# Kernel optimization log

Hardware: AMD Instinct MI355X
Metric: run time of the kernel (lower is better)

## Reference

```python
import jax, jax.numpy as jnp
import numpy as np
from jax import lax


def setup_inputs() -> dict:
    key = jax.random.key(0)
    ks = jax.random.split(key, 6)
    B, L, D, H, K = 32, 256, 16, 64, 5
    T = L - K + 1            # 252
    S = (T // 2) * H         # 8064
    return {
        "x": jax.random.normal(ks[0], (B, L, D), dtype=jnp.float32),
        "conv_w": jax.random.normal(ks[1], (D, H, K), dtype=jnp.float32) * 0.1,
        "conv_b": jax.random.normal(ks[2], (D, H), dtype=jnp.float32) * 0.1,
        "deconv_w": jax.random.normal(ks[3], (D, H, K), dtype=jnp.float32) * 0.1,
        "deconv_b": jax.random.normal(ks[4], (D,), dtype=jnp.float32) * 0.1,
        "W_attn": jax.random.normal(ks[5], (S, S), dtype=jnp.float32) * 0.01,
    }


def reference(x, conv_w, conv_b, deconv_w, deconv_b, W_attn):
    B, L, D = x.shape
    _, H, K = conv_w.shape
    T = L - K + 1
    P = T // 2
    S = P * H

    xt = jnp.transpose(x, (0, 2, 1))  # [B, D, L]
    # per-channel Conv1d(1->H) as one grouped conv: kernel [D*H, 1, K], groups=D
    y = lax.conv_general_dilated(
        xt, conv_w.reshape(D * H, 1, K), (1,), "VALID",
        dimension_numbers=("NCH", "OIH", "NCH"), feature_group_count=D,
    ) + conv_b.reshape(1, D * H, 1)
    y = jax.nn.relu(y)  # [B, D*H, T]

    # per-channel ConvTranspose1d(H->1) == full conv with flipped kernel, groups=D
    recon = lax.conv_general_dilated(
        y, deconv_w[..., ::-1], (1,), [(K - 1, K - 1)],
        dimension_numbers=("NCH", "OIH", "NCH"), feature_group_count=D,
    ) + deconv_b.reshape(1, D, 1)  # [B, D, L]

    # AvgPool1d(kernel=2, stride=2) then flatten(H, P) per channel
    pooled = y.reshape(B, D, H, P, 2).mean(axis=-1)  # [B, D, H, P]
    flat = pooled.reshape(B, D, S)                   # [B, D, S]

    main = flat[:, 0]        # [B, S]
    aux = flat[:, 1:]        # [B, D-1, S]

    # 'general' score: main . (aux @ W^T)  ==  (main @ W) . aux
    m = main @ W_attn                              # [B, S]
    scores = jnp.einsum("bt,bdt->bd", m, aux)      # [B, D-1]
    attn = jax.nn.softmax(scores, axis=-1)         # [B, D-1]
    weighted = jnp.einsum("bd,bds->bs", attn, aux)  # [B, S]

    out = jnp.concatenate([main[:, None, :], weighted[:, None, :]], axis=2)  # [B,1,2S]
    return out, attn[:, None, :], recon
```

## Files before the change

kernel.cpp:

```cpp
#include <hip/hip_runtime.h>
#include <math.h>

#define BB 32
#define LL 256
#define DD 16
#define HH 64
#define KK 5
#define TT 252
#define PP 126
#define SS 8064
#define NCHUNK 12
#define CHUNK 672
#define NKT 21

typedef __attribute__((ext_vector_type(8))) short bf16x8;
typedef __attribute__((ext_vector_type(4))) float f32x4;

__device__ __forceinline__ unsigned short f2bf(float f) {
  unsigned int u = __float_as_uint(f);
  u += 0x7FFFu + ((u >> 16) & 1u);
  return (unsigned short)(u >> 16);
}
__device__ __forceinline__ float bf2f(unsigned short h) {
  return __uint_as_float(((unsigned int)h) << 16);
}

__global__ __launch_bounds__(256) void k12_conv_recon(
    const float* __restrict__ x, const float* __restrict__ cw,
    const float* __restrict__ cb, const float* __restrict__ dw,
    const float* __restrict__ db, float* __restrict__ flat,
    unsigned short* __restrict__ mainH, unsigned short* __restrict__ mainL,
    float* __restrict__ recon) {
  __shared__ float ylds[HH * TT];
  __shared__ float xs[LL];
  __shared__ float cws[HH * KK];
  __shared__ float dws[HH * KK];
  __shared__ float cbs[HH];

  int bd = blockIdx.x;
  int b = bd / DD, d = bd % DD;
  int tid = threadIdx.x;

  xs[tid] = x[((size_t)b * LL + tid) * DD + d];
  for (int i = tid; i < HH * KK; i += 256) {
    cws[i] = cw[(size_t)d * HH * KK + i];
    dws[i] = dw[(size_t)d * HH * KK + i];
  }
  if (tid < HH) cbs[tid] = cb[d * HH + tid];
  __syncthreads();

  {
    int h = tid >> 2, a = tid & 3;
    int t0 = a * 63;
    float w0 = cws[h * KK + 0], w1 = cws[h * KK + 1], w2 = cws[h * KK + 2],
          w3 = cws[h * KK + 3], w4 = cws[h * KK + 4];
    float bias = cbs[h];
    float x0 = xs[t0], x1 = xs[t0 + 1], x2 = xs[t0 + 2], x3 = xs[t0 + 3],
          x4 = xs[t0 + 4];
    float* yrow = ylds + h * TT + t0;
    #pragma unroll 7
    for (int t = 0; t < 63; ++t) {
      float yv = fmaf(w4, x4, fmaf(w3, x3, fmaf(w2, x2, fmaf(w1, x1, fmaf(w0, x0, bias)))));
      yrow[t] = fmaxf(yv, 0.f);
      x0 = x1; x1 = x2; x2 = x3; x3 = x4;
      if (t < 62) x4 = xs[t0 + t + 5];
    }
  }
  __syncthreads();

  for (int i = tid; i < HH * PP; i += 256) {
    int h = i / PP, p = i - h * PP;
    float pooled = 0.5f * (ylds[h * TT + 2 * p] + ylds[h * TT + 2 * p + 1]);
    flat[(size_t)bd * SS + i] = pooled;
    if (d == 0) {
      unsigned short hb = f2bf(pooled);
      mainH[(size_t)b * SS + i] = hb;
      mainL[(size_t)b * SS + i] = f2bf(pooled - bf2f(hb));
    }
  }

  {
    int l = tid;
    float acc = db[d];
    for (int h = 0; h < HH; ++h) {
      const float* yl = ylds + h * TT;
      #pragma unroll
      for (int j = 0; j < KK; ++j) {
        int t = l - j;
        if (t >= 0 && t < TT) acc = fmaf(yl[t], dws[h * KK + j], acc);
      }
    }
    recon[(size_t)bd * LL + l] = acc;
  }
}

__global__ __launch_bounds__(256) void k3_mfma(
    const float* __restrict__ W, const unsigned short* __restrict__ mainH,
    const unsigned short* __restrict__ mainL, float* __restrict__ partial) {
  __shared__ unsigned short AH[4 * 32 * 8];
  __shared__ unsigned short AL[4 * 32 * 8];
  __shared__ unsigned short BH[4 * 64 * 8];
  __shared__ unsigned short BL[4 * 64 * 8];

  int tid = threadIdx.x;
  int chunk = blockIdx.y;
  int s0 = chunk * CHUNK;
  int cb = blockIdx.x * 64;

  int lane = tid & 63;
  int wv = tid >> 6;
  int mr = wv & 1;
  int nt0 = (wv >> 1) * 2;

  f32x4 acc0 = {0.f, 0.f, 0.f, 0.f};
  f32x4 acc1 = {0.f, 0.f, 0.f, 0.f};

  int sc = tid & 63;
  int sg = tid >> 6;

  int aoff = (lane >> 4) * 256 + ((lane & 15) + 16 * mr) * 8;
  int b0off = (lane >> 4) * 512 + ((lane & 15) + 16 * nt0) * 8;
  int b1off = b0off + 16 * 8;

  #pragma unroll 1
  for (int kt = 0; kt < NKT; ++kt) {
    const float* wsrc = W + (size_t)(s0 + kt * 32 + sg * 8) * SS + cb + sc;
    bf16x8 vh, vl;
    #pragma unroll
    for (int j = 0; j < 8; ++j) {
      float f = wsrc[(size_t)j * SS];
      unsigned short h = f2bf(f);
      float rem = f - bf2f(h);
      vh[j] = (short)h;
      vl[j] = (short)f2bf(rem);
    }
    *(bf16x8*)&BH[sg * 512 + sc * 8] = vh;
    *(bf16x8*)&BL[sg * 512 + sc * 8] = vl;
    if (tid < 128) {
      int ab = tid >> 2;
      int aq = tid & 3;
      size_t off = (size_t)ab * SS + (size_t)(s0 + kt * 32 + aq * 8);
      *(bf16x8*)&AH[aq * 256 + ab * 8] = *(const bf16x8*)(mainH + off);
      *(bf16x8*)&AL[aq * 256 + ab * 8] = *(const bf16x8*)(mainL + off);
    }
    __syncthreads();
    bf16x8 ah = *(const bf16x8*)&AH[aoff];
    bf16x8 al = *(const bf16x8*)&AL[aoff];
    bf16x8 b0h = *(const bf16x8*)&BH[b0off];
    bf16x8 b0l = *(const bf16x8*)&BL[b0off];
    bf16x8 b1h = *(const bf16x8*)&BH[b1off];
    bf16x8 b1l = *(const bf16x8*)&BL[b1off];
    acc0 = __builtin_amdgcn_mfma_f32_16x16x32_bf16(ah, b0h, acc0, 0, 0, 0);
    acc0 = __builtin_amdgcn_mfma_f32_16x16x32_bf16(ah, b0l, acc0, 0, 0, 0);
    acc0 = __builtin_amdgcn_mfma_f32_16x16x32_bf16(al, b0h, acc0, 0, 0, 0);
    acc1 = __builtin_amdgcn_mfma_f32_16x16x32_bf16(ah, b1h, acc1, 0, 0, 0);
    acc1 = __builtin_amdgcn_mfma_f32_16x16x32_bf16(ah, b1l, acc1, 0, 0, 0);
    acc1 = __builtin_amdgcn_mfma_f32_16x16x32_bf16(al, b1h, acc1, 0, 0, 0);
    __syncthreads();
  }

  int row0 = mr * 16 + (lane >> 4) * 4;
  int col0 = cb + nt0 * 16 + (lane & 15);
  float* pp = partial + ((size_t)chunk * BB + row0) * SS + col0;
  pp[0 * (size_t)SS] = acc0[0];
  pp[1 * (size_t)SS] = acc0[1];
  pp[2 * (size_t)SS] = acc0[2];
  pp[3 * (size_t)SS] = acc0[3];
  pp += 16;
  pp[0 * (size_t)SS] = acc1[0];
  pp[1 * (size_t)SS] = acc1[1];
  pp[2 * (size_t)SS] = acc1[2];
  pp[3 * (size_t)SS] = acc1[3];
}

__global__ __launch_bounds__(256) void k3b_reduce(
    const float4* __restrict__ partial, float4* __restrict__ m) {
  int i = blockIdx.x * 256 + threadIdx.x;
  float4 s = make_float4(0.f, 0.f, 0.f, 0.f);
  #pragma unroll
  for (int c = 0; c < NCHUNK; ++c) {
    float4 v = partial[(size_t)c * (BB * SS / 4) + i];
    s.x += v.x; s.y += v.y; s.z += v.z; s.w += v.w;
  }
  m[i] = s;
}

__global__ __launch_bounds__(256) void k4_scores(
    const float* __restrict__ m, const float* __restrict__ flat,
    float* __restrict__ scores) {
  int bd = blockIdx.x;
  int b = bd / 15, dd = bd % 15;
  const float* mb = m + (size_t)b * SS;
  const float* ab = flat + ((size_t)b * DD + 1 + dd) * SS;
  float p = 0.f;
  for (int s = threadIdx.x; s < SS; s += 256) p = fmaf(mb[s], ab[s], p);
  #pragma unroll
  for (int o = 32; o; o >>= 1) p += __shfl_xor(p, o);
  __shared__ float red[4];
  if ((threadIdx.x & 63) == 0) red[threadIdx.x >> 6] = p;
  __syncthreads();
  if (threadIdx.x == 0) scores[bd] = red[0] + red[1] + red[2] + red[3];
}

__global__ __launch_bounds__(64) void k5_softmax(
    const float* __restrict__ scores, float* __restrict__ attn_out) {
  int b = blockIdx.x;
  int lane = threadIdx.x;
  float v = (lane < 15) ? scores[b * 15 + lane] : -INFINITY;
  float mx = v;
  #pragma unroll
  for (int o = 32; o; o >>= 1) mx = fmaxf(mx, __shfl_xor(mx, o));
  float e = (lane < 15) ? expf(v - mx) : 0.f;
  float sum = e;
  #pragma unroll
  for (int o = 32; o; o >>= 1) sum += __shfl_xor(sum, o);
  if (lane < 15) attn_out[b * 15 + lane] = e / sum;
}

__global__ __launch_bounds__(256) void k6_out(
    const float* __restrict__ flat, const float* __restrict__ attn,
    float* __restrict__ out) {
  int b = blockIdx.y;
  int s = blockIdx.x * 256 + threadIdx.x;
  if (s >= SS) return;
  const float* fb = flat + (size_t)b * DD * SS;
  out[(size_t)b * 2 * SS + s] = fb[s];
  float w = 0.f;
  #pragma unroll
  for (int d = 0; d < 15; ++d)
    w = fmaf(attn[b * 15 + d], fb[(size_t)(1 + d) * SS + s], w);
  out[(size_t)b * 2 * SS + SS + s] = w;
}

extern "C" void kernel_launch(void* const* d_in, const int* in_sizes, int n_in,
                              void* d_out, int out_size, void* d_ws, size_t ws_size,
                              hipStream_t stream) {
  const float* x        = (const float*)d_in[0];
  const float* conv_w   = (const float*)d_in[1];
  const float* conv_b   = (const float*)d_in[2];
  const float* deconv_w = (const float*)d_in[3];
  const float* deconv_b = (const float*)d_in[4];
  const float* W_attn   = (const float*)d_in[5];
  float* out = (float*)d_out;

  const size_t ATTN_OFF  = (size_t)BB * 2 * SS;
  const size_t RECON_OFF = ATTN_OFF + (size_t)BB * 15;

  float* ws      = (float*)d_ws;
  float* partial = ws;
  float* flat    = partial + (size_t)NCHUNK * BB * SS;
  unsigned short* mainH = (unsigned short*)(flat + (size_t)BB * DD * SS);
  unsigned short* mainL = mainH + (size_t)BB * SS;
  float* m       = (float*)(mainL + (size_t)BB * SS);
  float* scores  = m + (size_t)BB * SS;

  k12_conv_recon<<<dim3(BB * DD), dim3(256), 0, stream>>>(
      x, conv_w, conv_b, deconv_w, deconv_b, flat, mainH, mainL, out + RECON_OFF);

  k3_mfma<<<dim3(SS / 64, NCHUNK), dim3(256), 0, stream>>>(
      W_attn, mainH, mainL, partial);

  k3b_reduce<<<dim3((BB * SS / 4) / 256), dim3(256), 0, stream>>>(
      (const float4*)partial, (float4*)m);

  k4_scores<<<dim3(BB * 15), dim3(256), 0, stream>>>(m, flat, scores);

  k5_softmax<<<dim3(BB), dim3(64), 0, stream>>>(scores, out + ATTN_OFF);

  k6_out<<<dim3((SS + 255) / 256, BB), dim3(256), 0, stream>>>(
      flat, out + ATTN_OFF, out);
}
```

Baseline: 106.7 us.

## Double-buffer LDS and prefetch W tiles two steps ahead in MFMA GEMV kernel

Restructures the k3_mfma main loop into a software pipeline. The W and main tiles for step kt+2 are loaded into registers and the tile for kt+1 is converted and written into a second LDS buffer while MFMAs run on the current buffer, which removes one __syncthreads per iteration. The bf16 hi/lo split switches from round-to-nearest to truncation, which is cheaper but changes how the error is split between the two halves. It costs more LDS and registers to hold the in-flight tile.

```diff
diff --git a/kernel.cpp b/kernel.cpp
--- a/kernel.cpp
+++ b/kernel.cpp
@@ -97,15 +97,15 @@
 __global__ __launch_bounds__(256) void k3_mfma(
     const float* __restrict__ W, const unsigned short* __restrict__ mainH,
     const unsigned short* __restrict__ mainL, float* __restrict__ partial) {
-  __shared__ unsigned short AH[4 * 32 * 8];
-  __shared__ unsigned short AL[4 * 32 * 8];
-  __shared__ unsigned short BH[4 * 64 * 8];
-  __shared__ unsigned short BL[4 * 64 * 8];
+  __shared__ unsigned short AH[2][1024];
+  __shared__ unsigned short AL[2][1024];
+  __shared__ unsigned short BH[2][2048];
+  __shared__ unsigned short BL[2][2048];
 
   int tid = threadIdx.x;
   int chunk = blockIdx.y;
   int s0 = chunk * CHUNK;
-  int cb = blockIdx.x * 64;
+  int cbase = blockIdx.x * 64;
 
   int lane = tid & 63;
   int wv = tid >> 6;
@@ -118,49 +118,74 @@
   int sc = tid & 63;
   int sg = tid >> 6;
 
-  int aoff = (lane >> 4) * 256 + ((lane & 15) + 16 * mr) * 8;
+  int aoff  = (lane >> 4) * 256 + ((lane & 15) + 16 * mr) * 8;
   int b0off = (lane >> 4) * 512 + ((lane & 15) + 16 * nt0) * 8;
-  int b1off = b0off + 16 * 8;
+  int b1off = b0off + 128;
+
+  const float* wbase = W + (size_t)(s0 + sg * 8) * SS + cbase + sc;
+  int ab = tid >> 2, aq = tid & 3;
+  size_t abase = (size_t)ab * SS + (size_t)(s0 + aq * 8);
+
+  float f0, f1, f2, f3, f4, f5, f6, f7;
+  bf16x8 aHr, aLr;
+
+#define LOADW(KT) {                                                   \
+    const float* p_ = wbase + (size_t)(KT) * 32 * SS;                 \
+    f0 = p_[0];                f1 = p_[(size_t)SS];                   \
+    f2 = p_[2 * (size_t)SS];   f3 = p_[3 * (size_t)SS];               \
+    f4 = p_[4 * (size_t)SS];   f5 = p_[5 * (size_t)SS];               \
+    f6 = p_[6 * (size_t)SS];   f7 = p_[7 * (size_t)SS]; }
+
+#define LOADA(KT) if (tid < 128) {                                    \
+    aHr = *(const bf16x8*)(mainH + abase + (KT) * 32);                \
+    aLr = *(const bf16x8*)(mainL + abase + (KT) * 32); }
+
+#define SPLIT1(F, J) {                                                \
+    unsigned int u_ = __float_as_uint(F);                             \
+    vh[J] = (short)(u_ >> 16);                                        \
+    float rem_ = F - __uint_as_float(u_ & 0xFFFF0000u);               \
+    vl[J] = (short)(__float_as_uint(rem_) >> 16); }
+
+#define CVTW(BUF) {                                                   \
+    bf16x8 vh, vl;                                                    \
+    SPLIT1(f0, 0) SPLIT1(f1, 1) SPLIT1(f2, 2) SPLIT1(f3, 3)           \
+    SPLIT1(f4, 4) SPLIT1(f5, 5) SPLIT1(f6, 6) SPLIT1(f7, 7)           \
+    *(bf16x8*)&BH[BUF][sg * 512 + sc * 8] = vh;                       \
+    *(bf16x8*)&BL[BUF][sg * 512 + sc * 8] = vl; }
+
+#define WRITEA(BUF) if (tid < 128) {                                  \
+    *(bf16x8*)&AH[BUF][aq * 256 + ab * 8] = aHr;                      \
+    *(bf16x8*)&AL[BUF][aq * 256 + ab * 8] = aLr; }
+
+#define DOMFMA(BUF) {                                                 \
+    bf16x8 ah  = *(const bf16x8*)&AH[BUF][aoff];                      \
+    bf16x8 al  = *(const bf16x8*)&AL[BUF][aoff];                      \
+    bf16x8 b0h = *(const bf16x8*)&BH[BUF][b0off];                     \
+    bf16x8 b0l = *(const bf16x8*)&BL[BUF][b0off];                     \
+    bf16x8 b1h = *(const bf16x8*)&BH[BUF][b1off];                     \
+    bf16x8 b1l = *(const bf16x8*)&BL[BUF][b1off];                     \
+    acc0 = __builtin_amdgcn_mfma_f32_16x16x32_bf16(ah, b0h, acc0, 0, 0, 0); \
+    acc0 = __builtin_amdgcn_mfma_f32_16x16x32_bf16(ah, b0l, acc0, 0, 0, 0); \
+    acc0 = __builtin_amdgcn_mfma_f32_16x16x32_bf16(al, b0h, acc0, 0, 0, 0); \
+    acc1 = __builtin_amdgcn_mfma_f32_16x16x32_bf16(ah, b1h, acc1, 0, 0, 0); \
+    acc1 = __builtin_amdgcn_mfma_f32_16x16x32_bf16(ah, b1l, acc1, 0, 0, 0); \
+    acc1 = __builtin_amdgcn_mfma_f32_16x16x32_bf16(al, b1h, acc1, 0, 0, 0); }
+
+  LOADW(0) LOADA(0)
+  CVTW(0) WRITEA(0)
+  LOADW(1) LOADA(1)
+  __syncthreads();
 
   #pragma unroll 1
   for (int kt = 0; kt < NKT; ++kt) {
-    const float* wsrc = W + (size_t)(s0 + kt * 32 + sg * 8) * SS + cb + sc;
-    bf16x8 vh, vl;
-    #pragma unroll
-    for (int j = 0; j < 8; ++j) {
-      float f = wsrc[(size_t)j * SS];
-      unsigned short h = f2bf(f);
-      float rem = f - bf2f(h);
-      vh[j] = (short)h;
-      vl[j] = (short)f2bf(rem);
-    }
-    *(bf16x8*)&BH[sg * 512 + sc * 8] = vh;
-    *(bf16x8*)&BL[sg * 512 + sc * 8] = vl;
-    if (tid < 128) {
-      int ab = tid >> 2;
-      int aq = tid & 3;
-      size_t off = (size_t)ab * SS + (size_t)(s0 + kt * 32 + aq * 8);
-      *(bf16x8*)&AH[aq * 256 + ab * 8] = *(const bf16x8*)(mainH + off);
-      *(bf16x8*)&AL[aq * 256 + ab * 8] = *(const bf16x8*)(mainL + off);
-    }
+    DOMFMA(kt & 1)
+    if (kt + 1 < NKT) { CVTW((kt + 1) & 1) WRITEA((kt + 1) & 1) }
+    if (kt + 2 < NKT) { LOADW(kt + 2) LOADA(kt + 2) }
     __syncthreads();
-    bf16x8 ah = *(const bf16x8*)&AH[aoff];
-    bf16x8 al = *(const bf16x8*)&AL[aoff];
-    bf16x8 b0h = *(const bf16x8*)&BH[b0off];
-    bf16x8 b0l = *(const bf16x8*)&BL[b0off];
-    bf16x8 b1h = *(const bf16x8*)&BH[b1off];
-    bf16x8 b1l = *(const bf16x8*)&BL[b1off];
-    acc0 = __builtin_amdgcn_mfma_f32_16x16x32_bf16(ah, b0h, acc0, 0, 0, 0);
-    acc0 = __builtin_amdgcn_mfma_f32_16x16x32_bf16(ah, b0l, acc0, 0, 0, 0);
-    acc0 = __builtin_amdgcn_mfma_f32_16x16x32_bf16(al, b0h, acc0, 0, 0, 0);
-    acc1 = __builtin_amdgcn_mfma_f32_16x16x32_bf16(ah, b1h, acc1, 0, 0, 0);
-    acc1 = __builtin_amdgcn_mfma_f32_16x16x32_bf16(ah, b1l, acc1, 0, 0, 0);
-    acc1 = __builtin_amdgcn_mfma_f32_16x16x32_bf16(al, b1h, acc1, 0, 0, 0);
-    __syncthreads();
   }
 
   int row0 = mr * 16 + (lane >> 4) * 4;
-  int col0 = cb + nt0 * 16 + (lane & 15);
+  int col0 = cbase + nt0 * 16 + (lane & 15);
   float* pp = partial + ((size_t)chunk * BB + row0) * SS + col0;
   pp[0 * (size_t)SS] = acc0[0];
   pp[1 * (size_t)SS] = acc0[1];
@@ -171,6 +196,12 @@
   pp[1 * (size_t)SS] = acc1[1];
   pp[2 * (size_t)SS] = acc1[2];
   pp[3 * (size_t)SS] = acc1[3];
+#undef LOADW
+#undef LOADA
+#undef SPLIT1
+#undef CVTW
+#undef WRITEA
+#undef DOMFMA
 }
 
 __global__ __launch_bounds__(256) void k3b_reduce(
```

Result: faster. 101.0 us (-5.4%).

## Rewrite GEMV-style matmul as LDS-free per-wave 32x32 MFMA with register pipelining

Applied to the files above, without the earlier changes.

Each wavefront now owns a 32-column by 384-row slice of W and loads its operands straight from global memory into registers, removing the shared-memory staging and both block barriers per step. It switches to 32x32x16 bf16 MFMAs and software-pipelines loads three steps deep. The bf16 hi/lo split of W becomes truncation instead of round-to-nearest, which is cheaper and keeps the three-product split accurate. The split-K count grows from 12 to 21 chunks, so the reduce kernel reads more partial sums.

```diff
diff --git a/kernel.cpp b/kernel.cpp
--- a/kernel.cpp
+++ b/kernel.cpp
@@ -9,12 +9,13 @@
 #define TT 252
 #define PP 126
 #define SS 8064
-#define NCHUNK 12
-#define CHUNK 672
-#define NKT 21
+#define NCHUNK 21
+#define CHUNK 384
+#define NSTEP 24
+#define NCT 252
 
 typedef __attribute__((ext_vector_type(8))) short bf16x8;
-typedef __attribute__((ext_vector_type(4))) float f32x4;
+typedef __attribute__((ext_vector_type(16))) float f32x16;
 
 __device__ __forceinline__ unsigned short f2bf(float f) {
   unsigned int u = __float_as_uint(f);
@@ -97,80 +98,75 @@
 __global__ __launch_bounds__(256) void k3_mfma(
     const float* __restrict__ W, const unsigned short* __restrict__ mainH,
     const unsigned short* __restrict__ mainL, float* __restrict__ partial) {
-  __shared__ unsigned short AH[4 * 32 * 8];
-  __shared__ unsigned short AL[4 * 32 * 8];
-  __shared__ unsigned short BH[4 * 64 * 8];
-  __shared__ unsigned short BL[4 * 64 * 8];
-
   int tid = threadIdx.x;
-  int chunk = blockIdx.y;
+  int lane = tid & 63;
+  int wid = blockIdx.x * 4 + (tid >> 6);
+  int ct = wid % NCT;
+  int chunk = wid / NCT;
+  int n0 = ct * 32;
   int s0 = chunk * CHUNK;
-  int cb = blockIdx.x * 64;
-
-  int lane = tid & 63;
-  int wv = tid >> 6;
-  int mr = wv & 1;
-  int nt0 = (wv >> 1) * 2;
-
-  f32x4 acc0 = {0.f, 0.f, 0.f, 0.f};
-  f32x4 acc1 = {0.f, 0.f, 0.f, 0.f};
-
-  int sc = tid & 63;
-  int sg = tid >> 6;
-
-  int aoff = (lane >> 4) * 256 + ((lane & 15) + 16 * mr) * 8;
-  int b0off = (lane >> 4) * 512 + ((lane & 15) + 16 * nt0) * 8;
-  int b1off = b0off + 16 * 8;
+  int colq = lane & 31;
+  int koct = lane >> 5;
+
+  const float* wb = W + (size_t)(s0 + koct * 8) * SS + n0 + colq;
+  const unsigned short* aHb = mainH + (size_t)colq * SS + s0 + koct * 8;
+  const unsigned short* aLb = mainL + (size_t)colq * SS + s0 + koct * 8;
+
+  f32x16 acc;
+  #pragma unroll
+  for (int r = 0; r < 16; ++r) acc[r] = 0.f;
+
+  float wA0, wA1, wA2, wA3, wA4, wA5, wA6, wA7;
+  float wB0, wB1, wB2, wB3, wB4, wB5, wB6, wB7;
+  float wC0, wC1, wC2, wC3, wC4, wC5, wC6, wC7;
+  bf16x8 aHA, aLA, aHB, aLB, aHC, aLC;
+
+#define LOADS(P, AHR, ALR, T) {                                       \
+    int tc_ = (T) < NSTEP ? (T) : NSTEP - 1;                          \
+    const float* p_ = wb + (size_t)tc_ * 16 * SS;                     \
+    P##0 = p_[0];                P##1 = p_[(size_t)SS];               \
+    P##2 = p_[2 * (size_t)SS];   P##3 = p_[3 * (size_t)SS];           \
+    P##4 = p_[4 * (size_t)SS];   P##5 = p_[5 * (size_t)SS];           \
+    P##6 = p_[6 * (size_t)SS];   P##7 = p_[7 * (size_t)SS];           \
+    AHR = *(const bf16x8*)(aHb + tc_ * 16);                           \
+    ALR = *(const bf16x8*)(aLb + tc_ * 16); }
+
+#define SPL(F, J) {                                                   \
+    unsigned int u_ = __float_as_uint(F);                             \
+    bh[J] = (short)(u_ >> 16);                                        \
+    float r_ = F - __uint_as_float(u_ & 0xFFFF0000u);                 \
+    bl[J] = (short)(__float_as_uint(r_) >> 16); }
+
+#define CONSUME(P, AHR, ALR) {                                        \
+    bf16x8 bh, bl;                                                    \
+    SPL(P##0, 0) SPL(P##1, 1) SPL(P##2, 2) SPL(P##3, 3)               \
+    SPL(P##4, 4) SPL(P##5, 5) SPL(P##6, 6) SPL(P##7, 7)               \
+    acc = __builtin_amdgcn_mfma_f32_32x32x16_bf16(AHR, bh, acc, 0, 0, 0); \
+    acc = __builtin_amdgcn_mfma_f32_32x32x16_bf16(AHR, bl, acc, 0, 0, 0); \
+    acc = __builtin_amdgcn_mfma_f32_32x32x16_bf16(ALR, bh, acc, 0, 0, 0); }
+
+  LOADS(wA, aHA, aLA, 0)
+  LOADS(wB, aHB, aLB, 1)
 
   #pragma unroll 1
-  for (int kt = 0; kt < NKT; ++kt) {
-    const float* wsrc = W + (size_t)(s0 + kt * 32 + sg * 8) * SS + cb + sc;
-    bf16x8 vh, vl;
-    #pragma unroll
-    for (int j = 0; j < 8; ++j) {
-      float f = wsrc[(size_t)j * SS];
-      unsigned short h = f2bf(f);
-      float rem = f - bf2f(h);
-      vh[j] = (short)h;
-      vl[j] = (short)f2bf(rem);
-    }
-    *(bf16x8*)&BH[sg * 512 + sc * 8] = vh;
-    *(bf16x8*)&BL[sg * 512 + sc * 8] = vl;
-    if (tid < 128) {
-      int ab = tid >> 2;
-      int aq = tid & 3;
-      size_t off = (size_t)ab * SS + (size_t)(s0 + kt * 32 + aq * 8);
-      *(bf16x8*)&AH[aq * 256 + ab * 8] = *(const bf16x8*)(mainH + off);
-      *(bf16x8*)&AL[aq * 256 + ab * 8] = *(const bf16x8*)(mainL + off);
-    }
-    __syncthreads();
-    bf16x8 ah = *(const bf16x8*)&AH[aoff];
-    bf16x8 al = *(const bf16x8*)&AL[aoff];
-    bf16x8 b0h = *(const bf16x8*)&BH[b0off];
-    bf16x8 b0l = *(const bf16x8*)&BL[b0off];
-    bf16x8 b1h = *(const bf16x8*)&BH[b1off];
-    bf16x8 b1l = *(const bf16x8*)&BL[b1off];
-    acc0 = __builtin_amdgcn_mfma_f32_16x16x32_bf16(ah, b0h, acc0, 0, 0, 0);
-    acc0 = __builtin_amdgcn_mfma_f32_16x16x32_bf16(ah, b0l, acc0, 0, 0, 0);
-    acc0 = __builtin_amdgcn_mfma_f32_16x16x32_bf16(al, b0h, acc0, 0, 0, 0);
-    acc1 = __builtin_amdgcn_mfma_f32_16x16x32_bf16(ah, b1h, acc1, 0, 0, 0);
-    acc1 = __builtin_amdgcn_mfma_f32_16x16x32_bf16(ah, b1l, acc1, 0, 0, 0);
-    acc1 = __builtin_amdgcn_mfma_f32_16x16x32_bf16(al, b1h, acc1, 0, 0, 0);
-    __syncthreads();
-  }
-
-  int row0 = mr * 16 + (lane >> 4) * 4;
-  int col0 = cb + nt0 * 16 + (lane & 15);
-  float* pp = partial + ((size_t)chunk * BB + row0) * SS + col0;
-  pp[0 * (size_t)SS] = acc0[0];
-  pp[1 * (size_t)SS] = acc0[1];
-  pp[2 * (size_t)SS] = acc0[2];
-  pp[3 * (size_t)SS] = acc0[3];
-  pp += 16;
-  pp[0 * (size_t)SS] = acc1[0];
-  pp[1 * (size_t)SS] = acc1[1];
-  pp[2 * (size_t)SS] = acc1[2];
-  pp[3 * (size_t)SS] = acc1[3];
+  for (int t = 0; t < NSTEP; t += 3) {
+    LOADS(wC, aHC, aLC, t + 2)
+    CONSUME(wA, aHA, aLA)
+    LOADS(wA, aHA, aLA, t + 3)
+    CONSUME(wB, aHB, aLB)
+    LOADS(wB, aHB, aLB, t + 4)
+    CONSUME(wC, aHC, aLC)
+  }
+
+  float* pp = partial + (size_t)chunk * BB * SS + n0 + colq;
+  #pragma unroll
+  for (int r = 0; r < 16; ++r) {
+    int row = (r & 3) + 8 * (r >> 2) + 4 * koct;
+    pp[(size_t)row * SS] = acc[r];
+  }
+#undef LOADS
+#undef SPL
+#undef CONSUME
 }
 
 __global__ __launch_bounds__(256) void k3b_reduce(
@@ -257,7 +253,7 @@
   k12_conv_recon<<<dim3(BB * DD), dim3(256), 0, stream>>>(
       x, conv_w, conv_b, deconv_w, deconv_b, flat, mainH, mainL, out + RECON_OFF);
 
-  k3_mfma<<<dim3(SS / 64, NCHUNK), dim3(256), 0, stream>>>(
+  k3_mfma<<<dim3((NCT * NCHUNK) / 4), dim3(256), 0, stream>>>(
       W_attn, mainH, mainL, partial);
 
   k3b_reduce<<<dim3((BB * SS / 4) / 256), dim3(256), 0, stream>>>(
```

After: 126.6 us. 18.6% more time.
